# Optimization experiments

Hardware: AMD Instinct MI355X
Metric: run time of the kernel (lower is better)

The kernel has to match this reference:

```python
import jax, jax.numpy as jnp
import numpy as np

NUM_BINS = 10
NUM_CLASSES = 128
ALPHA = 0.999
LABEL_SMOOTHING = 0.0


def setup_inputs() -> dict:
    key = jax.random.key(0)
    k1, k2, k3 = jax.random.split(key, 3)
    B, T, C = 16, 4096, NUM_CLASSES
    return {
        "pred_logits": jax.random.normal(k1, (B, T, C), dtype=jnp.float32),
        "target_prob": jax.random.uniform(k2, (B, T, C), dtype=jnp.float32),
        "mask": jax.random.uniform(k3, (B, T, 1), dtype=jnp.float32),
        "GD_stat_ema": jnp.ones((NUM_BINS,), dtype=jnp.float32),
        "label_stat_ema_each_class": jnp.ones((NUM_CLASSES * 3,), dtype=jnp.float32),
    }


def _bce_with_logits(x, t):
    # numerically stable BCEWithLogitsLoss, reduction='none'
    return jnp.maximum(x, 0.0) - x * t + jnp.log1p(jnp.exp(-jnp.abs(x)))


def _update_ema(ema, hist, num_bins):
    hist = hist / jnp.maximum(hist.sum(), 1e-10) * num_bins
    ema = ema * ALPHA + (1.0 - ALPHA) * hist
    return ema / jnp.maximum(ema.sum(), 1e-10) * num_bins


def reference(pred_logits, target_prob, mask, GD_stat_ema, label_stat_ema_each_class):
    m = jnp.broadcast_to(mask, pred_logits.shape)
    tp = jnp.clip(target_prob, LABEL_SMOOTHING, 1.0 - LABEL_SMOOTHING)

    raw_loss = _bce_with_logits(pred_logits, tp)
    pred_prob = jax.nn.sigmoid(pred_logits)
    grad_mag = jnp.abs(pred_prob - tp)

    bin_idx = jnp.clip(jnp.floor(grad_mag * NUM_BINS).astype(jnp.int32), 0, NUM_BINS - 1)
    GD_weights = 1.0 / jax.lax.stop_gradient(GD_stat_ema[bin_idx])

    # per-class 3-way probability bin: idx in [0, 3*num_classes)
    tpi = jnp.clip(jnp.floor(tp * 3.0).astype(jnp.int32), 0, 2) + 3 * jnp.arange(NUM_CLASSES, dtype=jnp.int32)
    classes_weights = 1.0 / jax.lax.stop_gradient(label_stat_ema_each_class[tpi])

    weights = jnp.sqrt(GD_weights * classes_weights)
    loss = (raw_loss * weights * m).sum() / jnp.maximum(m.sum(), 1e-10)

    # weighted histograms (bincount with float weights)
    GD_hist = jnp.zeros((NUM_BINS,), dtype=jnp.float32).at[bin_idx.ravel()].add(m.ravel())
    label_hist = jnp.zeros((NUM_CLASSES * 3,), dtype=jnp.float32).at[tpi.ravel()].add(m.ravel())

    GD_ema_new = _update_ema(GD_stat_ema, GD_hist, NUM_BINS)
    label_ema_new = _update_ema(label_stat_ema_each_class, label_hist, NUM_CLASSES * 3)
    return loss, GD_ema_new, label_ema_new
```

## Files before the change

kernel.cpp:

```cpp
#include <hip/hip_runtime.h>

#define NBINS 10
#define LBINS 384
#define NOUT  395
#define PSTRIDE 400
#define BLOCK 256

#define SGRID 1024
#define OUTER 2
#define BATCH 4
#define SGSTR (SGRID * BLOCK)

__global__ __launch_bounds__(256) void ghm_main_s(
    const float* __restrict__ xg, const float* __restrict__ tg,
    const float* __restrict__ mask,
    const float* __restrict__ gd_ema, const float* __restrict__ lab_ema,
    float* __restrict__ ws)
{
    __shared__ float s_rsgd[NBINS];
    __shared__ float s_rslab[LBINS];
    __shared__ float s_out[PSTRIDE];
    __shared__ float s_red[4];

    const int tid = threadIdx.x;
    if (tid < NBINS) s_rsgd[tid] = __builtin_amdgcn_rsqf(gd_ema[tid]);
    for (int i = tid; i < LBINS; i += BLOCK) s_rslab[i] = __builtin_amdgcn_rsqf(lab_ema[i]);
    for (int i = tid; i < PSTRIDE; i += BLOCK) s_out[i] = 0.f;
    __syncthreads();

    const int c0 = (tid & 31) * 4;
    float wl[4][3];
#pragma unroll
    for (int j = 0; j < 4; ++j)
#pragma unroll
        for (int t = 0; t < 3; ++t) wl[j][t] = s_rslab[(c0 + j) * 3 + t];

    float lab[4][3] = {{0.f}};
    float gdl[NBINS];
#pragma unroll
    for (int b = 0; b < NBINS; ++b) gdl[b] = 0.f;
    float loss_acc = 0.f;

    const float4* x4 = (const float4*)xg;
    const float4* t4 = (const float4*)tg;
    const int i0 = blockIdx.x * BLOCK + tid;

#pragma unroll
    for (int o = 0; o < OUTER; ++o) {
        float4 xv[BATCH], tv[BATCH]; float mv[BATCH];
#pragma unroll
        for (int k = 0; k < BATCH; ++k) {
            const int i = i0 + (o * BATCH + k) * SGSTR;
            xv[k] = x4[i];
            tv[k] = t4[i];
            mv[k] = mask[i >> 5];
        }
#pragma unroll
        for (int k = 0; k < BATCH; ++k) {
            const float m = mv[k];
            const float xs[4] = {xv[k].x, xv[k].y, xv[k].z, xv[k].w};
            const float ts[4] = {tv[k].x, tv[k].y, tv[k].z, tv[k].w};
            unsigned pack = 0u;
#pragma unroll
            for (int j = 0; j < 4; ++j) {
                const float x  = xs[j];
                const float tp = ts[j];
                const float E  = __expf(-fabsf(x));
                const float z  = 1.f + E;
                const float raw = fmaxf(x, 0.f) - x * tp + __logf(z);
                const float inv = __builtin_amdgcn_rcpf(z);
                const float tps = (x >= 0.f) ? tp : 1.f - tp;
                const float g   = fabsf(inv - tps);
                int bin = (int)(g * 10.f);  bin = bin > 9 ? 9 : bin;
                int t3  = (int)(tp * 3.f);  t3  = t3 > 2 ? 2 : t3;
                const float wlj = (t3 == 0) ? wl[j][0] : ((t3 == 1) ? wl[j][1] : wl[j][2]);
                const float w = s_rsgd[bin] * wlj;
                loss_acc = fmaf(raw * m, w, loss_acc);
#pragma unroll
                for (int t = 0; t < 3; ++t) lab[j][t] += (t3 == t) ? m : 0.f;
                pack += 1u << (3 * bin);
            }
#pragma unroll
            for (int b = 0; b < NBINS; ++b)
                gdl[b] = fmaf(m, (float)((pack >> (3 * b)) & 7u), gdl[b]);
        }
    }

    const int lane = tid & 63, wv = tid >> 6;
    float v = loss_acc;
#pragma unroll
    for (int off = 32; off > 0; off >>= 1) v += __shfl_down(v, off);
    if (lane == 0) s_red[wv] = v;
#pragma unroll
    for (int b = 0; b < NBINS; ++b) {
        float g = gdl[b];
#pragma unroll
        for (int off = 32; off > 0; off >>= 1) g += __shfl_down(g, off);
        if (lane == 0) atomicAdd(&s_out[1 + b], g);
    }
#pragma unroll
    for (int j = 0; j < 4; ++j)
#pragma unroll
        for (int t = 0; t < 3; ++t)
            atomicAdd(&s_out[11 + (c0 + j) * 3 + t], lab[j][t]);
    __syncthreads();

    float* slot = ws + (size_t)blockIdx.x * PSTRIDE;
    if (tid == 0) slot[0] = s_red[0] + s_red[1] + s_red[2] + s_red[3];
    if (tid >= 1) slot[tid] = s_out[tid];
    if (tid < PSTRIDE - BLOCK) slot[BLOCK + tid] = s_out[BLOCK + tid];
}

__global__ __launch_bounds__(512) void ghm_fin_s(
    const float* __restrict__ ws,
    const float* __restrict__ gd_ema, const float* __restrict__ lab_ema,
    float* __restrict__ out)
{
    __shared__ float4 s4[512];
    __shared__ float  sv[PSTRIDE];
    __shared__ float  red[512];
    __shared__ float  s_sc[1];

    const int tid = threadIdx.x;
    const int sub = tid >> 7, q = tid & 127;

    float ax = 0.f, ay = 0.f, az = 0.f, aw = 0.f;
    if (q < PSTRIDE / 4) {
        const float4* p = (const float4*)ws + q;
#pragma unroll 4
        for (int b = sub; b < SGRID; b += 4) {
            float4 u = p[b * (PSTRIDE / 4)];
            ax += u.x; ay += u.y; az += u.z; aw += u.w;
        }
    }
    s4[tid] = make_float4(ax, ay, az, aw);
    __syncthreads();
    if (tid < PSTRIDE / 4) {
        float4 a = s4[tid], b4 = s4[tid + 128], c = s4[tid + 256], d = s4[tid + 384];
        sv[4 * tid + 0] = a.x + b4.x + c.x + d.x;
        sv[4 * tid + 1] = a.y + b4.y + c.y + d.y;
        sv[4 * tid + 2] = a.z + b4.z + c.z + d.z;
        sv[4 * tid + 3] = a.w + b4.w + c.w + d.w;
    }
    __syncthreads();

    if (tid == 0) {
        float ms = 0.f;
        for (int b = 0; b < NBINS; ++b) ms += sv[1 + b];
        const float inv_m = 1.f / fmaxf(ms, 1e-10f);
        s_sc[0] = inv_m;
        out[0] = sv[0] * inv_m;
        float ge[NBINS], gs = 0.f;
        for (int b = 0; b < NBINS; ++b) {
            ge[b] = gd_ema[b] * 0.999f + 0.001f * (sv[1 + b] * inv_m * (float)NBINS);
            gs += ge[b];
        }
        const float ig = 1.f / fmaxf(gs, 1e-10f);
        for (int b = 0; b < NBINS; ++b) out[1 + b] = ge[b] * ig * (float)NBINS;
    }
    __syncthreads();
    const float inv_m = s_sc[0];

    float e = 0.f;
    if (tid < LBINS)
        e = lab_ema[tid] * 0.999f + 0.001f * (sv[11 + tid] * inv_m * (float)LBINS);
    red[tid] = e;
    __syncthreads();
    for (int off = 256; off > 0; off >>= 1) {
        if (tid < off) red[tid] += red[tid + off];
        __syncthreads();
    }
    const float ie = (float)LBINS / fmaxf(red[0], 1e-10f);
    if (tid < LBINS) out[11 + tid] = e * ie;
}

#define NSLICE 8
#define SLICE_STRIDE 512
#define AGRID 2048
#define AITER 4
#define AGSTR (AGRID * BLOCK)

__global__ __launch_bounds__(256, 3) void ghm_main_a(
    const float* __restrict__ xg, const float* __restrict__ tg,
    const float* __restrict__ mask,
    const float* __restrict__ gd_ema, const float* __restrict__ lab_ema,
    float* __restrict__ ws)
{
    __shared__ float s_rsgd[NBINS];
    __shared__ float s_rslab[LBINS];
    __shared__ float s_hlab[LBINS];
    __shared__ float s_hgd[NBINS];
    __shared__ float s_red[4];

    const int tid = threadIdx.x;
    if (tid < NBINS) { s_rsgd[tid] = __builtin_amdgcn_rsqf(gd_ema[tid]); s_hgd[tid] = 0.f; }
    for (int i = tid; i < LBINS; i += BLOCK) {
        s_rslab[i] = __builtin_amdgcn_rsqf(lab_ema[i]);
        s_hlab[i]  = 0.f;
    }
    __syncthreads();

    const int c0 = (tid & 31) * 4;
    float wl[4][3];
#pragma unroll
    for (int j = 0; j < 4; ++j)
#pragma unroll
        for (int t = 0; t < 3; ++t) wl[j][t] = s_rslab[(c0 + j) * 3 + t];

    float lab[4][3] = {{0.f}};
    float gdl[NBINS];
#pragma unroll
    for (int b = 0; b < NBINS; ++b) gdl[b] = 0.f;
    float loss_acc = 0.f;

    const float4* x4 = (const float4*)xg;
    const float4* t4 = (const float4*)tg;
    const int i0 = blockIdx.x * BLOCK + tid;

    float4 xv[AITER], tv[AITER]; float mv[AITER];
#pragma unroll
    for (int k = 0; k < AITER; ++k) {
        const int i = i0 + k * AGSTR;
        xv[k] = x4[i]; tv[k] = t4[i]; mv[k] = mask[i >> 5];
    }
#pragma unroll
    for (int k = 0; k < AITER; ++k) {
        const float m = mv[k];
        const float xs[4] = {xv[k].x, xv[k].y, xv[k].z, xv[k].w};
        const float ts[4] = {tv[k].x, tv[k].y, tv[k].z, tv[k].w};
        unsigned pack = 0u;
#pragma unroll
        for (int j = 0; j < 4; ++j) {
            const float x  = xs[j];
            const float tp = ts[j];
            const float E  = __expf(-fabsf(x));
            const float z  = 1.f + E;
            const float raw = fmaxf(x, 0.f) - x * tp + __logf(z);
            const float inv = __builtin_amdgcn_rcpf(z);
            const float tps = (x >= 0.f) ? tp : 1.f - tp;
            const float g   = fabsf(inv - tps);
            int bin = (int)(g * 10.f);  bin = bin > 9 ? 9 : bin;
            int t3  = (int)(tp * 3.f);  t3  = t3 > 2 ? 2 : t3;
            const float wlj = (t3 == 0) ? wl[j][0] : ((t3 == 1) ? wl[j][1] : wl[j][2]);
            const float w = s_rsgd[bin] * wlj;
            loss_acc = fmaf(raw * m, w, loss_acc);
#pragma unroll
            for (int t = 0; t < 3; ++t) lab[j][t] += (t3 == t) ? m : 0.f;
            pack += 1u << (3 * bin);
        }
#pragma unroll
        for (int b = 0; b < NBINS; ++b)
            gdl[b] = fmaf(m, (float)((pack >> (3 * b)) & 7u), gdl[b]);
    }

    const int lane = tid & 63, wv = tid >> 6;
    float v = loss_acc;
#pragma unroll
    for (int off = 32; off > 0; off >>= 1) v += __shfl_down(v, off);
    if (lane == 0) s_red[wv] = v;
#pragma unroll
    for (int b = 0; b < NBINS; ++b) {
        float g = gdl[b];
#pragma unroll
        for (int off = 32; off > 0; off >>= 1) g += __shfl_down(g, off);
        if (lane == 0) atomicAdd(&s_hgd[b], g);
    }
#pragma unroll
    for (int j = 0; j < 4; ++j)
#pragma unroll
        for (int t = 0; t < 3; ++t)
            atomicAdd(&s_hlab[(c0 + j) * 3 + t], lab[j][t]);
    __syncthreads();

    float* wss = ws + (blockIdx.x & (NSLICE - 1)) * SLICE_STRIDE;
    if (tid == 0) atomicAdd(&wss[0], s_red[0] + s_red[1] + s_red[2] + s_red[3]);
    if (tid < NBINS) atomicAdd(&wss[1 + tid], s_hgd[tid]);
    for (int e = tid; e < LBINS; e += BLOCK) atomicAdd(&wss[1 + NBINS + e], s_hlab[e]);
}

__global__ __launch_bounds__(512) void ghm_fin_a(
    const float* __restrict__ ws,
    const float* __restrict__ gd_ema, const float* __restrict__ lab_ema,
    float* __restrict__ out)
{
    __shared__ float red[512];
    __shared__ float s_gde[NBINS];
    __shared__ float s_gesum;

    const int tid = threadIdx.x;
    float v = 0.f;
    if (tid < NOUT) {
#pragma unroll
        for (int s = 0; s < NSLICE; ++s) v += ws[s * SLICE_STRIDE + tid];
    }
    red[tid] = (tid >= 1 && tid < 1 + NBINS) ? v : 0.f;
    __syncthreads();
    for (int off = 256; off > 0; off >>= 1) {
        if (tid < off) red[tid] += red[tid + off];
        __syncthreads();
    }
    const float msum = red[0];
    __syncthreads();
    const float inv_m = 1.f / fmaxf(msum, 1e-10f);
    if (tid == 0) out[0] = v * inv_m;
    if (tid >= 1 && tid < 1 + NBINS) {
        float hn = v * inv_m * (float)NBINS;
        s_gde[tid - 1] = gd_ema[tid - 1] * 0.999f + 0.001f * hn;
    }
    __syncthreads();
    if (tid == 0) {
        float s = 0.f;
        for (int b = 0; b < NBINS; ++b) s += s_gde[b];
        s_gesum = s;
    }
    __syncthreads();
    if (tid >= 1 && tid < 1 + NBINS)
        out[tid] = s_gde[tid - 1] / fmaxf(s_gesum, 1e-10f) * (float)NBINS;

    float e = 0.f;
    if (tid >= 1 + NBINS && tid < NOUT) {
        float hn = v * inv_m * (float)LBINS;
        e = lab_ema[tid - 1 - NBINS] * 0.999f + 0.001f * hn;
    }
    red[tid] = e;
    __syncthreads();
    for (int off = 256; off > 0; off >>= 1) {
        if (tid < off) red[tid] += red[tid + off];
        __syncthreads();
    }
    const float esum = red[0];
    if (tid >= 1 + NBINS && tid < NOUT)
        out[tid] = e / fmaxf(esum, 1e-10f) * (float)LBINS;
}

extern "C" void kernel_launch(void* const* d_in, const int* in_sizes, int n_in,
                              void* d_out, int out_size, void* d_ws, size_t ws_size,
                              hipStream_t stream)
{
    const float* logits  = (const float*)d_in[0];
    const float* tprob   = (const float*)d_in[1];
    const float* mask    = (const float*)d_in[2];
    const float* gd_ema  = (const float*)d_in[3];
    const float* lab_ema = (const float*)d_in[4];
    float* out = (float*)d_out;
    float* ws  = (float*)d_ws;

    const size_t need = (size_t)SGRID * PSTRIDE * sizeof(float);
    if (ws_size >= need) {
        ghm_main_s<<<SGRID, BLOCK, 0, stream>>>(logits, tprob, mask, gd_ema, lab_ema, ws);
        ghm_fin_s<<<1, 512, 0, stream>>>(ws, gd_ema, lab_ema, out);
    } else {
        hipMemsetAsync(ws, 0, NSLICE * SLICE_STRIDE * sizeof(float), stream);
        ghm_main_a<<<AGRID, BLOCK, 0, stream>>>(logits, tprob, mask, gd_ema, lab_ema, ws);
        ghm_fin_a<<<1, 512, 0, stream>>>(ws, gd_ema, lab_ema, out);
    }
}
```

Before: 153.9 us.

## Split final partial reduction across 100 blocks and flatten main load batch

The single-block final reduction over 1024 per-block partial rows is replaced by a two-stage scheme. A 100-block kernel reduces one float4 column each across all partials into a small buffer, and a tiny single-block kernel then applies the EMA updates. The main kernel now issues all 8 loads per thread up front instead of two batches of 4, and gains a min-blocks-per-CU launch bound. The intent is to spread the serial tail reduction across many CUs and raise memory-level parallelism, at the cost of an extra kernel launch and more registers per thread.

```diff
diff --git a/kernel.cpp b/kernel.cpp
--- a/kernel.cpp
+++ b/kernel.cpp
@@ -4,14 +4,14 @@
 #define LBINS 384
 #define NOUT  395
 #define PSTRIDE 400
+#define PQ (PSTRIDE / 4)
 #define BLOCK 256
 
 #define SGRID 1024
-#define OUTER 2
-#define BATCH 4
+#define SBATCH 8
 #define SGSTR (SGRID * BLOCK)
 
-__global__ __launch_bounds__(256) void ghm_main_s(
+__global__ __launch_bounds__(256, 3) void ghm_main_s(
     const float* __restrict__ xg, const float* __restrict__ tg,
     const float* __restrict__ mask,
     const float* __restrict__ gd_ema, const float* __restrict__ lab_ema,
@@ -45,186 +45,17 @@
     const float4* t4 = (const float4*)tg;
     const int i0 = blockIdx.x * BLOCK + tid;
 
-#pragma unroll
-    for (int o = 0; o < OUTER; ++o) {
-        float4 xv[BATCH], tv[BATCH]; float mv[BATCH];
-#pragma unroll
-        for (int k = 0; k < BATCH; ++k) {
-            const int i = i0 + (o * BATCH + k) * SGSTR;
-            xv[k] = x4[i];
-            tv[k] = t4[i];
-            mv[k] = mask[i >> 5];
-        }
-#pragma unroll
-        for (int k = 0; k < BATCH; ++k) {
-            const float m = mv[k];
-            const float xs[4] = {xv[k].x, xv[k].y, xv[k].z, xv[k].w};
-            const float ts[4] = {tv[k].x, tv[k].y, tv[k].z, tv[k].w};
-            unsigned pack = 0u;
-#pragma unroll
-            for (int j = 0; j < 4; ++j) {
-                const float x  = xs[j];
-                const float tp = ts[j];
-                const float E  = __expf(-fabsf(x));
-                const float z  = 1.f + E;
-                const float raw = fmaxf(x, 0.f) - x * tp + __logf(z);
-                const float inv = __builtin_amdgcn_rcpf(z);
-                const float tps = (x >= 0.f) ? tp : 1.f - tp;
-                const float g   = fabsf(inv - tps);
-                int bin = (int)(g * 10.f);  bin = bin > 9 ? 9 : bin;
-                int t3  = (int)(tp * 3.f);  t3  = t3 > 2 ? 2 : t3;
-                const float wlj = (t3 == 0) ? wl[j][0] : ((t3 == 1) ? wl[j][1] : wl[j][2]);
-                const float w = s_rsgd[bin] * wlj;
-                loss_acc = fmaf(raw * m, w, loss_acc);
-#pragma unroll
-                for (int t = 0; t < 3; ++t) lab[j][t] += (t3 == t) ? m : 0.f;
-                pack += 1u << (3 * bin);
-            }
-#pragma unroll
-            for (int b = 0; b < NBINS; ++b)
-                gdl[b] = fmaf(m, (float)((pack >> (3 * b)) & 7u), gdl[b]);
-        }
-    }
-
-    const int lane = tid & 63, wv = tid >> 6;
-    float v = loss_acc;
-#pragma unroll
-    for (int off = 32; off > 0; off >>= 1) v += __shfl_down(v, off);
-    if (lane == 0) s_red[wv] = v;
-#pragma unroll
-    for (int b = 0; b < NBINS; ++b) {
-        float g = gdl[b];
-#pragma unroll
-        for (int off = 32; off > 0; off >>= 1) g += __shfl_down(g, off);
-        if (lane == 0) atomicAdd(&s_out[1 + b], g);
-    }
-#pragma unroll
-    for (int j = 0; j < 4; ++j)
-#pragma unroll
-        for (int t = 0; t < 3; ++t)
-            atomicAdd(&s_out[11 + (c0 + j) * 3 + t], lab[j][t]);
-    __syncthreads();
-
-    float* slot = ws + (size_t)blockIdx.x * PSTRIDE;
-    if (tid == 0) slot[0] = s_red[0] + s_red[1] + s_red[2] + s_red[3];
-    if (tid >= 1) slot[tid] = s_out[tid];
-    if (tid < PSTRIDE - BLOCK) slot[BLOCK + tid] = s_out[BLOCK + tid];
-}
-
-__global__ __launch_bounds__(512) void ghm_fin_s(
-    const float* __restrict__ ws,
-    const float* __restrict__ gd_ema, const float* __restrict__ lab_ema,
-    float* __restrict__ out)
-{
-    __shared__ float4 s4[512];
-    __shared__ float  sv[PSTRIDE];
-    __shared__ float  red[512];
-    __shared__ float  s_sc[1];
-
-    const int tid = threadIdx.x;
-    const int sub = tid >> 7, q = tid & 127;
-
-    float ax = 0.f, ay = 0.f, az = 0.f, aw = 0.f;
-    if (q < PSTRIDE / 4) {
-        const float4* p = (const float4*)ws + q;
-#pragma unroll 4
-        for (int b = sub; b < SGRID; b += 4) {
-            float4 u = p[b * (PSTRIDE / 4)];
-            ax += u.x; ay += u.y; az += u.z; aw += u.w;
-        }
-    }
-    s4[tid] = make_float4(ax, ay, az, aw);
-    __syncthreads();
-    if (tid < PSTRIDE / 4) {
-        float4 a = s4[tid], b4 = s4[tid + 128], c = s4[tid + 256], d = s4[tid + 384];
-        sv[4 * tid + 0] = a.x + b4.x + c.x + d.x;
-        sv[4 * tid + 1] = a.y + b4.y + c.y + d.y;
-        sv[4 * tid + 2] = a.z + b4.z + c.z + d.z;
-        sv[4 * tid + 3] = a.w + b4.w + c.w + d.w;
-    }
-    __syncthreads();
-
-    if (tid == 0) {
-        float ms = 0.f;
-        for (int b = 0; b < NBINS; ++b) ms += sv[1 + b];
-        const float inv_m = 1.f / fmaxf(ms, 1e-10f);
-        s_sc[0] = inv_m;
-        out[0] = sv[0] * inv_m;
-        float ge[NBINS], gs = 0.f;
-        for (int b = 0; b < NBINS; ++b) {
-            ge[b] = gd_ema[b] * 0.999f + 0.001f * (sv[1 + b] * inv_m * (float)NBINS);
-            gs += ge[b];
-        }
-        const float ig = 1.f / fmaxf(gs, 1e-10f);
-        for (int b = 0; b < NBINS; ++b) out[1 + b] = ge[b] * ig * (float)NBINS;
-    }
-    __syncthreads();
-    const float inv_m = s_sc[0];
-
-    float e = 0.f;
-    if (tid < LBINS)
-        e = lab_ema[tid] * 0.999f + 0.001f * (sv[11 + tid] * inv_m * (float)LBINS);
-    red[tid] = e;
-    __syncthreads();
-    for (int off = 256; off > 0; off >>= 1) {
-        if (tid < off) red[tid] += red[tid + off];
-        __syncthreads();
-    }
-    const float ie = (float)LBINS / fmaxf(red[0], 1e-10f);
-    if (tid < LBINS) out[11 + tid] = e * ie;
-}
-
-#define NSLICE 8
-#define SLICE_STRIDE 512
-#define AGRID 2048
-#define AITER 4
-#define AGSTR (AGRID * BLOCK)
-
-__global__ __launch_bounds__(256, 3) void ghm_main_a(
-    const float* __restrict__ xg, const float* __restrict__ tg,
-    const float* __restrict__ mask,
-    const float* __restrict__ gd_ema, const float* __restrict__ lab_ema,
-    float* __restrict__ ws)
-{
-    __shared__ float s_rsgd[NBINS];
-    __shared__ float s_rslab[LBINS];
-    __shared__ float s_hlab[LBINS];
-    __shared__ float s_hgd[NBINS];
-    __shared__ float s_red[4];
-
-    const int tid = threadIdx.x;
-    if (tid < NBINS) { s_rsgd[tid] = __builtin_amdgcn_rsqf(gd_ema[tid]); s_hgd[tid] = 0.f; }
-    for (int i = tid; i < LBINS; i += BLOCK) {
-        s_rslab[i] = __builtin_amdgcn_rsqf(lab_ema[i]);
-        s_hlab[i]  = 0.f;
-    }
-    __syncthreads();
-
-    const int c0 = (tid & 31) * 4;
-    float wl[4][3];
-#pragma unroll
-    for (int j = 0; j < 4; ++j)
-#pragma unroll
-        for (int t = 0; t < 3; ++t) wl[j][t] = s_rslab[(c0 + j) * 3 + t];
-
-    float lab[4][3] = {{0.f}};
-    float gdl[NBINS];
-#pragma unroll
-    for (int b = 0; b < NBINS; ++b) gdl[b] = 0.f;
-    float loss_acc = 0.f;
-
-    const float4* x4 = (const float4*)xg;
-    const float4* t4 = (const float4*)tg;
-    const int i0 = blockIdx.x * BLOCK + tid;
-
-    float4 xv[AITER], tv[AITER]; float mv[AITER];
-#pragma unroll
-    for (int k = 0; k < AITER; ++k) {
-        const int i = i0 + k * AGSTR;
-        xv[k] = x4[i]; tv[k] = t4[i]; mv[k] = mask[i >> 5];
-    }
-#pragma unroll
-    for (int k = 0; k < AITER; ++k) {
+    float4 xv[SBATCH], tv[SBATCH]; float mv[SBATCH];
+#pragma unroll
+    for (int k = 0; k < SBATCH; ++k) {
+        const int i = i0 + k * SGSTR;
+        xv[k] = x4[i];
+        tv[k] = t4[i];
+        mv[k] = mask[i >> 5];
+    }
+
+#pragma unroll
+    for (int k = 0; k < SBATCH; ++k) {
         const float m = mv[k];
         const float xs[4] = {xv[k].x, xv[k].y, xv[k].z, xv[k].w};
         const float ts[4] = {tv[k].x, tv[k].y, tv[k].z, tv[k].w};
@@ -263,6 +94,176 @@
         float g = gdl[b];
 #pragma unroll
         for (int off = 32; off > 0; off >>= 1) g += __shfl_down(g, off);
+        if (lane == 0) atomicAdd(&s_out[1 + b], g);
+    }
+#pragma unroll
+    for (int j = 0; j < 4; ++j)
+#pragma unroll
+        for (int t = 0; t < 3; ++t)
+            atomicAdd(&s_out[11 + (c0 + j) * 3 + t], lab[j][t]);
+    __syncthreads();
+
+    float* slot = ws + (size_t)blockIdx.x * PSTRIDE;
+    if (tid == 0) slot[0] = s_red[0] + s_red[1] + s_red[2] + s_red[3];
+    if (tid >= 1) slot[tid] = s_out[tid];
+    if (tid < PSTRIDE - BLOCK) slot[BLOCK + tid] = s_out[BLOCK + tid];
+}
+
+__global__ __launch_bounds__(256) void ghm_fin1(
+    const float* __restrict__ ws, float* __restrict__ ws2)
+{
+    __shared__ float4 r[BLOCK];
+    const int tid = threadIdx.x;
+    const float4* p = (const float4*)ws + blockIdx.x;
+    float4 a = make_float4(0.f, 0.f, 0.f, 0.f);
+    for (int b = tid; b < SGRID; b += BLOCK) {
+        float4 u = p[(size_t)b * PQ];
+        a.x += u.x; a.y += u.y; a.z += u.z; a.w += u.w;
+    }
+    r[tid] = a;
+    __syncthreads();
+    for (int off = BLOCK / 2; off > 0; off >>= 1) {
+        if (tid < off) {
+            float4 u = r[tid + off];
+            r[tid].x += u.x; r[tid].y += u.y; r[tid].z += u.z; r[tid].w += u.w;
+        }
+        __syncthreads();
+    }
+    if (tid == 0) ((float4*)ws2)[blockIdx.x] = r[0];
+}
+
+__global__ __launch_bounds__(512) void ghm_fin2(
+    const float* __restrict__ sv_g,
+    const float* __restrict__ gd_ema, const float* __restrict__ lab_ema,
+    float* __restrict__ out)
+{
+    __shared__ float sv[PSTRIDE];
+    __shared__ float red[512];
+    __shared__ float s_sc[1];
+
+    const int tid = threadIdx.x;
+    if (tid < PSTRIDE) sv[tid] = sv_g[tid];
+    __syncthreads();
+
+    if (tid == 0) {
+        float ms = 0.f;
+        for (int b = 0; b < NBINS; ++b) ms += sv[1 + b];
+        const float inv_m = 1.f / fmaxf(ms, 1e-10f);
+        s_sc[0] = inv_m;
+        out[0] = sv[0] * inv_m;
+        float ge[NBINS], gs = 0.f;
+        for (int b = 0; b < NBINS; ++b) {
+            ge[b] = gd_ema[b] * 0.999f + 0.001f * (sv[1 + b] * inv_m * (float)NBINS);
+            gs += ge[b];
+        }
+        const float ig = 1.f / fmaxf(gs, 1e-10f);
+        for (int b = 0; b < NBINS; ++b) out[1 + b] = ge[b] * ig * (float)NBINS;
+    }
+    __syncthreads();
+    const float inv_m = s_sc[0];
+
+    float e = 0.f;
+    if (tid < LBINS)
+        e = lab_ema[tid] * 0.999f + 0.001f * (sv[11 + tid] * inv_m * (float)LBINS);
+    red[tid] = e;
+    __syncthreads();
+    for (int off = 256; off > 0; off >>= 1) {
+        if (tid < off) red[tid] += red[tid + off];
+        __syncthreads();
+    }
+    const float ie = (float)LBINS / fmaxf(red[0], 1e-10f);
+    if (tid < LBINS) out[11 + tid] = e * ie;
+}
+
+#define NSLICE 8
+#define SLICE_STRIDE 512
+#define AGRID 2048
+#define AITER 4
+#define AGSTR (AGRID * BLOCK)
+
+__global__ __launch_bounds__(256, 3) void ghm_main_a(
+    const float* __restrict__ xg, const float* __restrict__ tg,
+    const float* __restrict__ mask,
+    const float* __restrict__ gd_ema, const float* __restrict__ lab_ema,
+    float* __restrict__ ws)
+{
+    __shared__ float s_rsgd[NBINS];
+    __shared__ float s_rslab[LBINS];
+    __shared__ float s_hlab[LBINS];
+    __shared__ float s_hgd[NBINS];
+    __shared__ float s_red[4];
+
+    const int tid = threadIdx.x;
+    if (tid < NBINS) { s_rsgd[tid] = __builtin_amdgcn_rsqf(gd_ema[tid]); s_hgd[tid] = 0.f; }
+    for (int i = tid; i < LBINS; i += BLOCK) {
+        s_rslab[i] = __builtin_amdgcn_rsqf(lab_ema[i]);
+        s_hlab[i]  = 0.f;
+    }
+    __syncthreads();
+
+    const int c0 = (tid & 31) * 4;
+    float wl[4][3];
+#pragma unroll
+    for (int j = 0; j < 4; ++j)
+#pragma unroll
+        for (int t = 0; t < 3; ++t) wl[j][t] = s_rslab[(c0 + j) * 3 + t];
+
+    float lab[4][3] = {{0.f}};
+    float gdl[NBINS];
+#pragma unroll
+    for (int b = 0; b < NBINS; ++b) gdl[b] = 0.f;
+    float loss_acc = 0.f;
+
+    const float4* x4 = (const float4*)xg;
+    const float4* t4 = (const float4*)tg;
+    const int i0 = blockIdx.x * BLOCK + tid;
+
+    float4 xv[AITER], tv[AITER]; float mv[AITER];
+#pragma unroll
+    for (int k = 0; k < AITER; ++k) {
+        const int i = i0 + k * AGSTR;
+        xv[k] = x4[i]; tv[k] = t4[i]; mv[k] = mask[i >> 5];
+    }
+#pragma unroll
+    for (int k = 0; k < AITER; ++k) {
+        const float m = mv[k];
+        const float xs[4] = {xv[k].x, xv[k].y, xv[k].z, xv[k].w};
+        const float ts[4] = {tv[k].x, tv[k].y, tv[k].z, tv[k].w};
+        unsigned pack = 0u;
+#pragma unroll
+        for (int j = 0; j < 4; ++j) {
+            const float x  = xs[j];
+            const float tp = ts[j];
+            const float E  = __expf(-fabsf(x));
+            const float z  = 1.f + E;
+            const float raw = fmaxf(x, 0.f) - x * tp + __logf(z);
+            const float inv = __builtin_amdgcn_rcpf(z);
+            const float tps = (x >= 0.f) ? tp : 1.f - tp;
+            const float g   = fabsf(inv - tps);
+            int bin = (int)(g * 10.f);  bin = bin > 9 ? 9 : bin;
+            int t3  = (int)(tp * 3.f);  t3  = t3 > 2 ? 2 : t3;
+            const float wlj = (t3 == 0) ? wl[j][0] : ((t3 == 1) ? wl[j][1] : wl[j][2]);
+            const float w = s_rsgd[bin] * wlj;
+            loss_acc = fmaf(raw * m, w, loss_acc);
+#pragma unroll
+            for (int t = 0; t < 3; ++t) lab[j][t] += (t3 == t) ? m : 0.f;
+            pack += 1u << (3 * bin);
+        }
+#pragma unroll
+        for (int b = 0; b < NBINS; ++b)
+            gdl[b] = fmaf(m, (float)((pack >> (3 * b)) & 7u), gdl[b]);
+    }
+
+    const int lane = tid & 63, wv = tid >> 6;
+    float v = loss_acc;
+#pragma unroll
+    for (int off = 32; off > 0; off >>= 1) v += __shfl_down(v, off);
+    if (lane == 0) s_red[wv] = v;
+#pragma unroll
+    for (int b = 0; b < NBINS; ++b) {
+        float g = gdl[b];
+#pragma unroll
+        for (int off = 32; off > 0; off >>= 1) g += __shfl_down(g, off);
         if (lane == 0) atomicAdd(&s_hgd[b], g);
     }
 #pragma unroll
@@ -345,10 +346,12 @@
     float* out = (float*)d_out;
     float* ws  = (float*)d_ws;
 
-    const size_t need = (size_t)SGRID * PSTRIDE * sizeof(float);
+    const size_t need = ((size_t)SGRID * PSTRIDE + PSTRIDE) * sizeof(float);
     if (ws_size >= need) {
+        float* ws2 = ws + (size_t)SGRID * PSTRIDE;
         ghm_main_s<<<SGRID, BLOCK, 0, stream>>>(logits, tprob, mask, gd_ema, lab_ema, ws);
-        ghm_fin_s<<<1, 512, 0, stream>>>(ws, gd_ema, lab_ema, out);
+        ghm_fin1<<<PQ, BLOCK, 0, stream>>>(ws, ws2);
+        ghm_fin2<<<1, 512, 0, stream>>>(ws2, gd_ema, lab_ema, out);
     } else {
         hipMemsetAsync(ws, 0, NSLICE * SLICE_STRIDE * sizeof(float), stream);
         ghm_main_a<<<AGRID, BLOCK, 0, stream>>>(logits, tprob, mask, gd_ema, lab_ema, ws);
```

New measurement: 166.9 us. 8.5% more time.
